# Kernel tuning notes

Measured on AMD Instinct MI355X. Metric: run time of the kernel, lower is better.

Reference implementation:

```python
import jax, jax.numpy as jnp
import numpy as np

L = 0.24        # diffusion step size (diffuse() default)
K = 0.03        # exp(logk) with logk = log(0.03) for feature_extractor='none'
EPS = 1e-8
NSTEPS = 128    # number of diffusion iterations (Npre)
SCALE = 4       # H/sh super-resolution factor (512/128)


def _g(x, k=K):
    return 1.0 / (1.0 + jnp.abs(x * x) / (k * k))


def _c(I, k=K):
    # I: [B, C, H, W] guide features; channel-mean abs finite differences -> edge-stopping coeffs
    cv = _g(jnp.mean(jnp.abs(I[:, :, 1:, :] - I[:, :, :-1, :]), axis=1, keepdims=True), k)  # [B,1,H-1,W]
    ch = _g(jnp.mean(jnp.abs(I[:, :, :, 1:] - I[:, :, :, :-1]), axis=1, keepdims=True), k)  # [B,1,H,W-1]
    return cv, ch


def _diffuse_step(cv, ch, I, l=L):
    # dv/dh computed from the ORIGINAL I (matches torch: both diffs taken before in-place updates,
    # and the in-place +/- updates commute since tv/th are fixed).
    dv = I[:, :, 1:, :] - I[:, :, :-1, :]
    dh = I[:, :, :, 1:] - I[:, :, :, :-1]
    tv = l * cv * dv
    th = l * ch * dh
    I = I.at[:, :, 1:, :].add(-tv).at[:, :, :-1, :].add(tv)
    I = I.at[:, :, :, 1:].add(-th).at[:, :, :, :-1].add(th)
    return I


def _adjust_step(img, source, mask_inv, eps=EPS):
    B, C, H, W = img.shape
    sh, sw = H // SCALE, W // SCALE
    # AdaptiveAvgPool2d((sh, sw)) with exact integer factor == block mean
    img_ss = img.reshape(B, C, sh, SCALE, sw, SCALE).mean(axis=(3, 5))
    ratio_ss = source / (img_ss + eps)
    ratio_ss = jnp.where(mask_inv, jnp.ones_like(ratio_ss), ratio_ss)
    # F.interpolate(mode='nearest') with exact integer factor == repeat
    ratio = jnp.repeat(jnp.repeat(ratio_ss, SCALE, axis=2), SCALE, axis=3)
    return img * ratio


def _diffuse(img, guide, source, mask_inv):
    guide_feats = jnp.concatenate([img, guide], axis=1)  # feature_extractor='none' path
    cv, ch = _c(guide_feats, K)

    def step(I, _):
        I = _diffuse_step(cv, ch, I, L)
        I = _adjust_step(I, source, mask_inv, EPS)
        return I, None

    img, _ = jax.lax.scan(step, img, None, length=NSTEPS)
    return img, cv, ch


def setup_inputs() -> dict:
    key = jax.random.key(0)
    k1, k2, k3, k4 = jax.random.split(key, 4)
    guide = jax.random.normal(k1, (2, 3, 512, 512), dtype=jnp.float32)
    # depth values kept positive and > deps=0.1 so the shift branch in forward() is not taken
    y_bicubic = jax.random.uniform(k2, (2, 1, 512, 512), dtype=jnp.float32) + 0.5
    source = jax.random.uniform(k3, (2, 1, 128, 128), dtype=jnp.float32) + 0.5
    mask_lr = jax.random.uniform(k4, (2, 1, 128, 128), dtype=jnp.float32)
    return {"guide": guide, "y_bicubic": y_bicubic, "source": source, "mask_lr": mask_lr}


def reference(guide, y_bicubic, source, mask_lr):
    mask_inv = mask_lr > 0.5
    y_pred, cv, ch = _diffuse(y_bicubic, guide, source, mask_inv)
    return y_pred, cv, ch
```

## Files before the change

### kernel.cpp

```cpp
#include <hip/hip_runtime.h>

constexpr int Hh = 512, Ww = 512, Bn = 2;
constexpr int SWs = 128;
constexpr float Lf = 0.24f;
constexpr float Kf = 0.03f;
constexpr float EPSf = 1e-8f;
constexpr int NSTEPS = 128;

constexpr int NPIX = Bn * Hh * Ww;
constexpr int CVN  = Bn * (Hh - 1) * Ww;

constexpr int OT = 32;
constexpr int KS = 7;
constexpr int HALO = 4 * KS;
constexpr int G = (OT + 2 * HALO) / 4;
constexpr int NB = G * G;
constexpr int NTHR = 512;
constexpr int REC = 20;
constexpr int NWG = Bn * (Hh / OT) * (Ww / OT);

__device__ __forceinline__ int clampi(int v, int lo, int hi) {
  return min(max(v, lo), hi);
}
__device__ __forceinline__ int recof(int t) { return t * REC; }

__global__ __launch_bounds__(256) void cvch_kernel(
    const float* __restrict__ img, const float* __restrict__ guide,
    float* __restrict__ cv, float* __restrict__ ch) {
  int idx = blockIdx.x * blockDim.x + threadIdx.x;
  if (idx >= NPIX) return;
  int x = idx & (Ww - 1);
  int y = (idx >> 9) & (Hh - 1);
  int b = idx >> 18;
  const float inv_k2 = 1.0f / (Kf * Kf);
  const float* f0 = img + (size_t)b * Hh * Ww;
  const float* g0 = guide + (size_t)b * 3 * Hh * Ww;
  const float* g1 = g0 + Hh * Ww;
  const float* g2 = g1 + Hh * Ww;
  int p = y * Ww + x;
  float c0 = f0[p], c1 = g0[p], c2 = g1[p], c3 = g2[p];
  if (y < Hh - 1) {
    int q = p + Ww;
    float m = (fabsf(f0[q] - c0) + fabsf(g0[q] - c1) +
               fabsf(g1[q] - c2) + fabsf(g2[q] - c3)) * 0.25f;
    cv[(b * (Hh - 1) + y) * Ww + x] = 1.0f / (1.0f + m * m * inv_k2);
  }
  if (x < Ww - 1) {
    int q = p + 1;
    float m = (fabsf(f0[q] - c0) + fabsf(g0[q] - c1) +
               fabsf(g1[q] - c2) + fabsf(g2[q] - c3)) * 0.25f;
    ch[(b * Hh + y) * (Ww - 1) + x] = 1.0f / (1.0f + m * m * inv_k2);
  }
}

__global__ __launch_bounds__(NTHR, 4) void diffuse7_kernel(
    const float* __restrict__ src, float* __restrict__ dst,
    const float* __restrict__ cv, const float* __restrict__ ch,
    const float* __restrict__ source, const float* __restrict__ mask,
    int nsteps) {
  __shared__ __align__(16) float ebuf[NB * REC];

  int wg = blockIdx.x;
  int b  = wg >> 8;
  int t  = wg & 255;
  int Ty0 = (t >> 4) * OT;
  int Tx0 = (t & 15) * OT;

  int tid = threadIdx.x;
  int tt = min(tid, NB - 1);
  int by = tt / G, bx = tt - by * G;
  int gy0 = Ty0 - HALO + 4 * by;
  int gx0 = Tx0 - HALO + 4 * bx;

  float* pMy = ebuf + recof(tt);
  const float* pU = ebuf + recof(by > 0     ? tt - G : tt) + 4;
  const float* pD = ebuf + recof(by < G - 1 ? tt + G : tt) + 0;
  const float* pL = ebuf + recof(bx > 0     ? tt - 1 : tt) + 12;
  const float* pR = ebuf + recof(bx < G - 1 ? tt + 1 : tt) + 8;

  const size_t ib = (size_t)b * Hh * Ww;
  const float* S = src + ib;
  float* D = dst + ib;
  const float* cvb = cv + (size_t)b * (Hh - 1) * Ww;
  const float* chb = ch + (size_t)b * Hh * (Ww - 1);

  auto ld4 = [&](int gy, int gx) -> float4 {
    gy = clampi(gy, 0, Hh - 1);
    if (gx < 0)      { float v = S[gy * Ww];          return make_float4(v, v, v, v); }
    if (gx > Ww - 4) { float v = S[gy * Ww + Ww - 1]; return make_float4(v, v, v, v); }
    return *reinterpret_cast<const float4*>(&S[gy * Ww + gx]);
  };

  float I[4][4];
#pragma unroll
  for (int r = 0; r < 4; ++r) {
    float4 t4 = ld4(gy0 + r, gx0);
    I[r][0] = t4.x; I[r][1] = t4.y; I[r][2] = t4.z; I[r][3] = t4.w;
  }
  float nT[4], nB[4], nL[4], nR[4];
  {
    float4 t4 = ld4(gy0 - 1, gx0);
    nT[0] = t4.x; nT[1] = t4.y; nT[2] = t4.z; nT[3] = t4.w;
    t4 = ld4(gy0 + 4, gx0);
    nB[0] = t4.x; nB[1] = t4.y; nB[2] = t4.z; nB[3] = t4.w;
    int cL = clampi(gx0 - 1, 0, Ww - 1), cR = clampi(gx0 + 4, 0, Ww - 1);
#pragma unroll
    for (int r = 0; r < 4; ++r) {
      int gy = clampi(gy0 + r, 0, Hh - 1);
      nL[r] = S[gy * Ww + cL];
      nR[r] = S[gy * Ww + cR];
    }
  }

  float cvk[5][4];
#pragma unroll
  for (int k = 0; k < 5; ++k) {
    int ro = gy0 - 1 + k;
    if (ro < 0 || ro > Hh - 2) {
      cvk[k][0] = cvk[k][1] = cvk[k][2] = cvk[k][3] = 0.0f;
    } else if (gx0 < 0) {
      float v = Lf * cvb[ro * Ww];
      cvk[k][0] = cvk[k][1] = cvk[k][2] = cvk[k][3] = v;
    } else if (gx0 > Ww - 4) {
      float v = Lf * cvb[ro * Ww + Ww - 1];
      cvk[k][0] = cvk[k][1] = cvk[k][2] = cvk[k][3] = v;
    } else {
      float4 t4 = *reinterpret_cast<const float4*>(&cvb[ro * Ww + gx0]);
      cvk[k][0] = Lf * t4.x; cvk[k][1] = Lf * t4.y;
      cvk[k][2] = Lf * t4.z; cvk[k][3] = Lf * t4.w;
    }
  }
  float chk[4][5];
#pragma unroll
  for (int r = 0; r < 4; ++r) {
    int ri = clampi(gy0 + r, 0, Hh - 1);
#pragma unroll
    for (int j = 0; j < 5; ++j) {
      int e = gx0 - 1 + j;
      chk[r][j] = (e >= 0 && e <= Ww - 2) ? Lf * chb[ri * (Ww - 1) + e] : 0.0f;
    }
  }

  int sy = clampi(gy0 >> 2, 0, SWs - 1);
  int sx = clampi(gx0 >> 2, 0, SWs - 1);
  int sidx = (b * SWs + sy) * SWs + sx;
  float srcv = source[sidx];
  bool mskv = mask[sidx] > 0.5f;

#pragma unroll
  for (int s = 0; s < KS; ++s) {
    if (s >= nsteps) break;
    if (s > 0) {
      __syncthreads();
      float4 t4;
      t4 = *reinterpret_cast<const float4*>(pU);
      nT[0] = t4.x; nT[1] = t4.y; nT[2] = t4.z; nT[3] = t4.w;
      t4 = *reinterpret_cast<const float4*>(pD);
      nB[0] = t4.x; nB[1] = t4.y; nB[2] = t4.z; nB[3] = t4.w;
      t4 = *reinterpret_cast<const float4*>(pL);
      nL[0] = t4.x; nL[1] = t4.y; nL[2] = t4.z; nL[3] = t4.w;
      t4 = *reinterpret_cast<const float4*>(pR);
      nR[0] = t4.x; nR[1] = t4.y; nR[2] = t4.z; nR[3] = t4.w;
    }

    float sum = 0.0f;
    float rowOrig[4];
#pragma unroll
    for (int r = 0; r < 4; ++r) {
      float leftOrig = 0.0f;
#pragma unroll
      for (int c = 0; c < 4; ++c) {
        float cc = I[r][c];
        float up = (r == 0) ? nT[c] : rowOrig[c];
        float dn = (r == 3) ? nB[c] : I[r + 1][c];
        float lf = (c == 0) ? nL[r] : leftOrig;
        float rt = (c == 3) ? nR[r] : I[r][c + 1];
        float acc = cc + cvk[r + 1][c] * (dn - cc) - cvk[r][c] * (cc - up)
                       + chk[r][c + 1] * (rt - cc) - chk[r][c] * (cc - lf);
        rowOrig[c] = cc;
        leftOrig = cc;
        I[r][c] = acc;
        sum += acc;
      }
    }
    float ratio = mskv ? 1.0f : srcv / (sum * 0.0625f + EPSf);
#pragma unroll
    for (int r = 0; r < 4; ++r)
#pragma unroll
      for (int c = 0; c < 4; ++c) I[r][c] *= ratio;

    if (s == nsteps - 1) {
      if (by >= KS && by < G - KS && bx >= KS && bx < G - KS) {
#pragma unroll
        for (int r = 0; r < 4; ++r)
          *reinterpret_cast<float4*>(&D[(gy0 + r) * Ww + gx0]) =
              make_float4(I[r][0], I[r][1], I[r][2], I[r][3]);
      }
    } else {
      __syncthreads();
      if (by > s && by < G - 1 - s && bx > s && bx < G - 1 - s) {
        *reinterpret_cast<float4*>(pMy + 0) =
            make_float4(I[0][0], I[0][1], I[0][2], I[0][3]);
        *reinterpret_cast<float4*>(pMy + 4) =
            make_float4(I[3][0], I[3][1], I[3][2], I[3][3]);
        *reinterpret_cast<float4*>(pMy + 8) =
            make_float4(I[0][0], I[1][0], I[2][0], I[3][0]);
        *reinterpret_cast<float4*>(pMy + 12) =
            make_float4(I[0][3], I[1][3], I[2][3], I[3][3]);
      }
    }
  }
}

constexpr int FT = 32;
__global__ __launch_bounds__(64) void step_kernel(
    const float* __restrict__ src, float* __restrict__ dst,
    const float* __restrict__ cv, const float* __restrict__ ch,
    const float* __restrict__ source, const float* __restrict__ mask) {
  __shared__ float sIl[FT + 2][FT + 3];
  int b = blockIdx.z;
  int ty0 = blockIdx.y * FT, tx0 = blockIdx.x * FT;
  const float* I = src + (size_t)b * Hh * Ww;
  int tid = threadIdx.x;
  for (int i = tid; i < (FT + 2) * (FT + 2); i += 64) {
    int ly = i / (FT + 2), lx = i % (FT + 2);
    int gy = max(0, min(Hh - 1, ty0 + ly - 1));
    int gx = max(0, min(Ww - 1, tx0 + lx - 1));
    sIl[ly][lx] = I[gy * Ww + gx];
  }
  __syncthreads();
  int bby = tid >> 3, bbx = tid & 7;
  int py0 = bby * 4, px0 = bbx * 4;
  int gy0 = ty0 + py0, gx0 = tx0 + px0;
  const float* cvb = cv + (size_t)b * (Hh - 1) * Ww;
  const float* chb = ch + (size_t)b * Hh * (Ww - 1);
  float v[4][4]; float sum = 0.0f;
#pragma unroll
  for (int dy = 0; dy < 4; ++dy) {
    int y = gy0 + dy, ly = py0 + dy + 1;
#pragma unroll
    for (int dx = 0; dx < 4; ++dx) {
      int x = gx0 + dx, lx = px0 + dx + 1;
      float cc = sIl[ly][lx];
      float acc = cc;
      if (y < Hh - 1) acc += Lf * cvb[y * Ww + x] * (sIl[ly + 1][lx] - cc);
      if (y > 0)      acc -= Lf * cvb[(y - 1) * Ww + x] * (cc - sIl[ly - 1][lx]);
      if (x < Ww - 1) acc += Lf * chb[y * (Ww - 1) + x] * (sIl[ly][lx + 1] - cc);
      if (x > 0)      acc -= Lf * chb[y * (Ww - 1) + x - 1] * (cc - sIl[ly][lx - 1]);
      v[dy][dx] = acc; sum += acc;
    }
  }
  int sidx = (b * SWs + (gy0 >> 2)) * SWs + (gx0 >> 2);
  float ratio = (mask[sidx] > 0.5f) ? 1.0f : source[sidx] / (sum * 0.0625f + EPSf);
  float* D = dst + (size_t)b * Hh * Ww;
#pragma unroll
  for (int dy = 0; dy < 4; ++dy)
    *reinterpret_cast<float4*>(&D[(gy0 + dy) * Ww + gx0]) =
        make_float4(v[dy][0] * ratio, v[dy][1] * ratio,
                    v[dy][2] * ratio, v[dy][3] * ratio);
}

extern "C" void kernel_launch(void* const* d_in, const int* in_sizes, int n_in,
                              void* d_out, int out_size, void* d_ws, size_t ws_size,
                              hipStream_t stream) {
  const float* guide  = (const float*)d_in[0];
  const float* ybic   = (const float*)d_in[1];
  const float* source = (const float*)d_in[2];
  const float* mask   = (const float*)d_in[3];

  float* out   = (float*)d_out;
  float* ypred = out;
  float* cv    = out + NPIX;
  float* ch    = out + NPIX + CVN;

  cvch_kernel<<<dim3((NPIX + 255) / 256), dim3(256), 0, stream>>>(ybic, guide, cv, ch);

  if (ws_size >= (size_t)2 * NPIX * sizeof(float)) {
    float* wsb0 = (float*)d_ws;
    float* wsb1 = wsb0 + NPIX;
    const float* sp = ybic;
    int done = 0, l = 0;
    while (done < NSTEPS) {
      int ns = (NSTEPS - done >= KS) ? KS : (NSTEPS - done);
      bool lastL = (done + ns == NSTEPS);
      float* dp = lastL ? ypred : ((l & 1) ? wsb1 : wsb0);
      diffuse7_kernel<<<dim3(NWG), dim3(NTHR), 0, stream>>>(sp, dp, cv, ch,
                                                            source, mask, ns);
      sp = dp; done += ns; ++l;
    }
  } else {
    float* wsbuf = (float*)d_ws;
    dim3 grid(Ww / FT, Hh / FT, Bn);
    const float* sp = ybic;
    for (int it = 0; it < NSTEPS; ++it) {
      float* dp = (it & 1) ? ypred : wsbuf;
      step_kernel<<<grid, dim3(64), 0, stream>>>(sp, dp, cv, ch, source, mask);
      sp = dp;
    }
  }
}
```

Before: 371.6 us.

## Fuse eight diffusion steps per launch with fp16-packed coefficients and trimmed halo ring

Temporal blocking depth goes from 7 to 8 steps per launch, so 128 steps take exactly 16 launches instead of 19, with less global traffic and launch overhead. The outermost ring of 4x4 blocks is no longer given a thread; neighbours at the trimmed edge fall back to their own record, which stays correct because those halo blocks are discarded by the final write. This keeps 484 active threads within 512 even though the halo grew. The cv/ch edge coefficients are packed into half2 registers to relieve register pressure at four blocks per SM, at the cost of fp16 rounding of the coefficients.

```diff
diff --git a/kernel.cpp b/kernel.cpp
--- a/kernel.cpp
+++ b/kernel.cpp
@@ -1,4 +1,5 @@
 #include <hip/hip_runtime.h>
+#include <hip/hip_fp16.h>
 
 constexpr int Hh = 512, Ww = 512, Bn = 2;
 constexpr int SWs = 128;
@@ -11,13 +12,15 @@
 constexpr int CVN  = Bn * (Hh - 1) * Ww;
 
 constexpr int OT = 32;
-constexpr int KS = 7;
+constexpr int KS = 8;
 constexpr int HALO = 4 * KS;
 constexpr int G = (OT + 2 * HALO) / 4;
-constexpr int NB = G * G;
+constexpr int GI = G - 2;
+constexpr int NB = GI * GI;
 constexpr int NTHR = 512;
 constexpr int REC = 20;
 constexpr int NWG = Bn * (Hh / OT) * (Ww / OT);
+constexpr int NLAUNCH = NSTEPS / KS;
 
 __device__ __forceinline__ int clampi(int v, int lo, int hi) {
   return min(max(v, lo), hi);
@@ -53,11 +56,10 @@
   }
 }
 
-__global__ __launch_bounds__(NTHR, 4) void diffuse7_kernel(
+__global__ __launch_bounds__(NTHR, 4) void diffuse8_kernel(
     const float* __restrict__ src, float* __restrict__ dst,
     const float* __restrict__ cv, const float* __restrict__ ch,
-    const float* __restrict__ source, const float* __restrict__ mask,
-    int nsteps) {
+    const float* __restrict__ source, const float* __restrict__ mask) {
   __shared__ __align__(16) float ebuf[NB * REC];
 
   int wg = blockIdx.x;
@@ -67,16 +69,18 @@
   int Tx0 = (t & 15) * OT;
 
   int tid = threadIdx.x;
+  bool own = tid < NB;
   int tt = min(tid, NB - 1);
-  int by = tt / G, bx = tt - by * G;
+  int iy = tt / GI, ix = tt - iy * GI;
+  int by = 1 + iy, bx = 1 + ix;
   int gy0 = Ty0 - HALO + 4 * by;
   int gx0 = Tx0 - HALO + 4 * bx;
 
   float* pMy = ebuf + recof(tt);
-  const float* pU = ebuf + recof(by > 0     ? tt - G : tt) + 4;
-  const float* pD = ebuf + recof(by < G - 1 ? tt + G : tt) + 0;
-  const float* pL = ebuf + recof(bx > 0     ? tt - 1 : tt) + 12;
-  const float* pR = ebuf + recof(bx < G - 1 ? tt + 1 : tt) + 8;
+  const float* pU = ebuf + recof(by > 1      ? tt - GI : tt) + 4;
+  const float* pD = ebuf + recof(by < G - 2  ? tt + GI : tt) + 0;
+  const float* pL = ebuf + recof(bx > 1      ? tt - 1  : tt) + 12;
+  const float* pR = ebuf + recof(bx < G - 2  ? tt + 1  : tt) + 8;
 
   const size_t ib = (size_t)b * Hh * Ww;
   const float* S = src + ib;
@@ -112,32 +116,49 @@
     }
   }
 
-  float cvk[5][4];
-#pragma unroll
-  for (int k = 0; k < 5; ++k) {
-    int ro = gy0 - 1 + k;
-    if (ro < 0 || ro > Hh - 2) {
-      cvk[k][0] = cvk[k][1] = cvk[k][2] = cvk[k][3] = 0.0f;
-    } else if (gx0 < 0) {
-      float v = Lf * cvb[ro * Ww];
-      cvk[k][0] = cvk[k][1] = cvk[k][2] = cvk[k][3] = v;
-    } else if (gx0 > Ww - 4) {
-      float v = Lf * cvb[ro * Ww + Ww - 1];
-      cvk[k][0] = cvk[k][1] = cvk[k][2] = cvk[k][3] = v;
-    } else {
-      float4 t4 = *reinterpret_cast<const float4*>(&cvb[ro * Ww + gx0]);
-      cvk[k][0] = Lf * t4.x; cvk[k][1] = Lf * t4.y;
-      cvk[k][2] = Lf * t4.z; cvk[k][3] = Lf * t4.w;
-    }
-  }
-  float chk[4][5];
-#pragma unroll
-  for (int r = 0; r < 4; ++r) {
-    int ri = clampi(gy0 + r, 0, Hh - 1);
-#pragma unroll
-    for (int j = 0; j < 5; ++j) {
-      int e = gx0 - 1 + j;
-      chk[r][j] = (e >= 0 && e <= Ww - 2) ? Lf * chb[ri * (Ww - 1) + e] : 0.0f;
+  __half2 cvp[2][4];
+  float cv4[4];
+  __half2 chp[4][2];
+  float ch4[4];
+  {
+    float ck[5][4];
+#pragma unroll
+    for (int k = 0; k < 5; ++k) {
+      int ro = gy0 - 1 + k;
+      if (ro < 0 || ro > Hh - 2) {
+        ck[k][0] = ck[k][1] = ck[k][2] = ck[k][3] = 0.0f;
+      } else if (gx0 < 0) {
+        float v = Lf * cvb[ro * Ww];
+        ck[k][0] = ck[k][1] = ck[k][2] = ck[k][3] = v;
+      } else if (gx0 > Ww - 4) {
+        float v = Lf * cvb[ro * Ww + Ww - 1];
+        ck[k][0] = ck[k][1] = ck[k][2] = ck[k][3] = v;
+      } else {
+        float4 t4 = *reinterpret_cast<const float4*>(&cvb[ro * Ww + gx0]);
+        ck[k][0] = Lf * t4.x; ck[k][1] = Lf * t4.y;
+        ck[k][2] = Lf * t4.z; ck[k][3] = Lf * t4.w;
+      }
+    }
+#pragma unroll
+    for (int c = 0; c < 4; ++c) {
+      cvp[0][c] = __floats2half2_rn(ck[0][c], ck[1][c]);
+      cvp[1][c] = __floats2half2_rn(ck[2][c], ck[3][c]);
+      cv4[c] = ck[4][c];
+    }
+  }
+  {
+#pragma unroll
+    for (int r = 0; r < 4; ++r) {
+      int ri = clampi(gy0 + r, 0, Hh - 1);
+      float cj[5];
+#pragma unroll
+      for (int j = 0; j < 5; ++j) {
+        int e = gx0 - 1 + j;
+        cj[j] = (e >= 0 && e <= Ww - 2) ? Lf * chb[ri * (Ww - 1) + e] : 0.0f;
+      }
+      chp[r][0] = __floats2half2_rn(cj[0], cj[1]);
+      chp[r][1] = __floats2half2_rn(cj[2], cj[3]);
+      ch4[r] = cj[4];
     }
   }
 
@@ -149,7 +170,6 @@
 
 #pragma unroll
   for (int s = 0; s < KS; ++s) {
-    if (s >= nsteps) break;
     if (s > 0) {
       __syncthreads();
       float4 t4;
@@ -170,13 +190,24 @@
       float leftOrig = 0.0f;
 #pragma unroll
       for (int c = 0; c < 4; ++c) {
+        float cu, cd;
+        if (r == 0)      { float2 u = __half22float2(cvp[0][c]); cu = u.x; cd = u.y; }
+        else if (r == 1) { cu = __high2float(cvp[0][c]); cd = __low2float(cvp[1][c]); }
+        else if (r == 2) { float2 u = __half22float2(cvp[1][c]); cu = u.x; cd = u.y; }
+        else             { cu = __high2float(cvp[1][c]); cd = cv4[c]; }
+        float cl, cr;
+        if (c == 0)      { float2 u = __half22float2(chp[r][0]); cl = u.x; cr = u.y; }
+        else if (c == 1) { cl = __high2float(chp[r][0]); cr = __low2float(chp[r][1]); }
+        else if (c == 2) { float2 u = __half22float2(chp[r][1]); cl = u.x; cr = u.y; }
+        else             { cl = __high2float(chp[r][1]); cr = ch4[r]; }
+
         float cc = I[r][c];
         float up = (r == 0) ? nT[c] : rowOrig[c];
         float dn = (r == 3) ? nB[c] : I[r + 1][c];
         float lf = (c == 0) ? nL[r] : leftOrig;
         float rt = (c == 3) ? nR[r] : I[r][c + 1];
-        float acc = cc + cvk[r + 1][c] * (dn - cc) - cvk[r][c] * (cc - up)
-                       + chk[r][c + 1] * (rt - cc) - chk[r][c] * (cc - lf);
+        float acc = cc + cd * (dn - cc) - cu * (cc - up)
+                       + cr * (rt - cc) - cl * (cc - lf);
         rowOrig[c] = cc;
         leftOrig = cc;
         I[r][c] = acc;
@@ -189,7 +220,7 @@
 #pragma unroll
       for (int c = 0; c < 4; ++c) I[r][c] *= ratio;
 
-    if (s == nsteps - 1) {
+    if (s == KS - 1) {
       if (by >= KS && by < G - KS && bx >= KS && bx < G - KS) {
 #pragma unroll
         for (int r = 0; r < 4; ++r)
@@ -198,7 +229,7 @@
       }
     } else {
       __syncthreads();
-      if (by > s && by < G - 1 - s && bx > s && bx < G - 1 - s) {
+      if (own && by > s && by < G - 1 - s && bx > s && bx < G - 1 - s) {
         *reinterpret_cast<float4*>(pMy + 0) =
             make_float4(I[0][0], I[0][1], I[0][2], I[0][3]);
         *reinterpret_cast<float4*>(pMy + 4) =
@@ -279,14 +310,11 @@
     float* wsb0 = (float*)d_ws;
     float* wsb1 = wsb0 + NPIX;
     const float* sp = ybic;
-    int done = 0, l = 0;
-    while (done < NSTEPS) {
-      int ns = (NSTEPS - done >= KS) ? KS : (NSTEPS - done);
-      bool lastL = (done + ns == NSTEPS);
-      float* dp = lastL ? ypred : ((l & 1) ? wsb1 : wsb0);
-      diffuse7_kernel<<<dim3(NWG), dim3(NTHR), 0, stream>>>(sp, dp, cv, ch,
-                                                            source, mask, ns);
-      sp = dp; done += ns; ++l;
+    for (int l = 0; l < NLAUNCH; ++l) {
+      float* dp = (l == NLAUNCH - 1) ? ypred : ((l & 1) ? wsb1 : wsb0);
+      diffuse8_kernel<<<dim3(NWG), dim3(NTHR), 0, stream>>>(sp, dp, cv, ch,
+                                                            source, mask);
+      sp = dp;
     }
   } else {
     float* wsbuf = (float*)d_ws;
```

Result: slower. 449.2 us (+20.9%).
